# Kernel tuning notes

Measured on AMD Instinct MI355X. Metric: run time of the kernel, lower is better.

## Reference

```python
import jax, jax.numpy as jnp
import numpy as np

B, T, D = 2, 2048, 1024
NH, DH = 16, 64
DD_PAIRS = DH // 4          # 16
DD_DIM = DD_PAIRS * 2      # 32
FFN = (D * 8 // 3 + 7) // 8 * 8  # 2736
EPS = 1e-6


def rms_norm(x, w):
    # torch nn.RMSNorm: x / sqrt(mean(x^2) + eps) * w over last dim
    var = jnp.mean(jnp.square(x), axis=-1, keepdims=True)
    return x * jax.lax.rsqrt(var + EPS) * w


def apply_rotary(x, cos, sin):
    d = x.shape[-1]
    x1, x2 = x[..., : d // 2], x[..., d // 2 :]
    return jnp.concatenate([x1 * cos - x2 * sin, x2 * cos + x1 * sin], axis=-1)


def setup_inputs() -> dict:
    key = jax.random.key(0)
    ks = jax.random.split(key, 10)
    s = 0.02  # small init scale so activations stay sane
    # fixed RoPE tables: (1, T, 1, DH//2)
    inv_freq = 1.0 / (10000.0 ** (jnp.arange(DH // 2, dtype=jnp.float32) / (DH // 2)))
    ang = jnp.arange(T, dtype=jnp.float32)[:, None] * inv_freq[None, :]  # (T, 32)
    rope_cos = jnp.cos(ang)[None, :, None, :]
    rope_sin = jnp.sin(ang)[None, :, None, :]
    return {
        "x": jax.random.normal(ks[0], (B, T, D), jnp.float32),
        "rope_cos": rope_cos,
        "rope_sin": rope_sin,
        "lerp_w": jax.random.normal(ks[1], (D, D), jnp.float32) * s,
        "lerp_b": jnp.full((D,), -2.0, jnp.float32),
        "attn_norm_w": jnp.ones((D,), jnp.float32),
        "w_qkv": jax.random.normal(ks[2], (3 * D, D), jnp.float32) * s,
        "q_norm_w": jnp.ones((DH,), jnp.float32),
        "k_norm_w": jnp.ones((DH,), jnp.float32),
        "q_post_bias": jnp.ones((DH,), jnp.float32),
        "k_post_bias": jnp.ones((DH,), jnp.float32),
        "dd_w": jax.random.normal(ks[3], (NH * DD_PAIRS, D), jnp.float32) * s,
        "dd_b": jnp.zeros((NH * DD_PAIRS,), jnp.float32),
        "w_o": jax.random.normal(ks[4], (D, D), jnp.float32) * s,
        "mlp_norm_w": jnp.ones((D,), jnp.float32),
        "gate_w": jax.random.normal(ks[5], (FFN, D), jnp.float32) * s,
        "up_w": jax.random.normal(ks[6], (FFN, D), jnp.float32) * s,
        "down_w": jax.random.normal(ks[7], (D, FFN), jnp.float32) * s,
    }


def reference(x, rope_cos, rope_sin, lerp_w, lerp_b, attn_norm_w, w_qkv,
              q_norm_w, k_norm_w, q_post_bias, k_post_bias, dd_w, dd_b,
              w_o, mlp_norm_w, gate_w, up_w, down_w):
    # CausalLerp: x[t] <- (1-g)*x[t] + g*x[t-1], content-gated
    x_prev = jnp.pad(x[:, :-1], ((0, 0), (1, 0), (0, 0)))
    g = jax.nn.sigmoid(x @ lerp_w.T + lerp_b)
    x = (1.0 - g) * x + g * x_prev

    # Attention branch
    h = rms_norm(x, attn_norm_w)
    qkv = (h @ w_qkv.T).reshape(B, T, 3, NH, DH)
    q, k, v = qkv[:, :, 0], qkv[:, :, 1], qkv[:, :, 2]  # (B,T,NH,DH)
    q = rms_norm(q, q_norm_w) * q_post_bias
    k = rms_norm(k, k_norm_w) * k_post_bias

    # DD-RoPE angles: cumsum of learned deltas over time
    dd_angles = (x @ dd_w.T + dd_b).reshape(B, T, NH, DD_PAIRS)
    dd_angles = jnp.cumsum(dd_angles, axis=1)
    dd_cos, dd_sin = jnp.cos(dd_angles), jnp.sin(dd_angles)

    fp = DD_DIM // 2  # 16
    def hybrid(qk):
        fixed = apply_rotary(qk[..., :DD_DIM], rope_cos[..., :fp], rope_sin[..., :fp])
        dd = apply_rotary(qk[..., DD_DIM:], dd_cos, dd_sin)
        return jnp.concatenate([fixed, dd], axis=-1)

    q, k = hybrid(q), hybrid(k)

    # causal SDPA
    scale = 1.0 / jnp.sqrt(jnp.float32(DH))
    scores = jnp.einsum("bihd,bjhd->bhij", q, k) * scale  # (B,NH,T,T)
    causal = jnp.tril(jnp.ones((T, T), bool))
    scores = jnp.where(causal, scores, jnp.float32(-1e30))
    attn = jax.nn.softmax(scores, axis=-1)
    y = jnp.einsum("bhij,bjhd->bihd", attn, v).reshape(B, T, D)
    x = x + y @ w_o.T

    # SwiGLU MLP
    h = rms_norm(x, mlp_norm_w)
    x = x + (jax.nn.silu(h @ gate_w.T) * (h @ up_w.T)) @ down_w.T
    return x
```

## Files before the change

kernel.cpp:

```cpp
#include <hip/hip_runtime.h>

typedef unsigned short u16;
typedef __attribute__((ext_vector_type(8))) short short8;
typedef __attribute__((ext_vector_type(4))) short short4v;
typedef __attribute__((ext_vector_type(4))) float f32x4;
typedef __attribute__((ext_vector_type(4))) unsigned short u16x4;

static constexpr int TB   = 2;
static constexpr int TT   = 2048;
static constexpr int TD   = 1024;
static constexpr int TNH  = 16;
static constexpr int TDH  = 64;
static constexpr int TFFN = 2736;
static constexpr int TFFNP= 2752;
static constexpr int TBT  = TB * TT;

#define DEVI static __device__ __forceinline__

typedef __attribute__((address_space(1))) const unsigned int gas_t;
typedef __attribute__((address_space(3))) unsigned int las_t;
#define GLOAD16(src, dst) __builtin_amdgcn_global_load_lds((gas_t*)(src), (las_t*)(dst), 16, 0, 0)

DEVI u16 f2bf(float f) {
  union { float f; unsigned u; } v; v.f = f;
  unsigned r = v.u + 0x7FFFu + ((v.u >> 16) & 1u);
  return (u16)(r >> 16);
}
DEVI float bf2f(u16 u) {
  union { unsigned u; float f; } v; v.u = ((unsigned)u) << 16;
  return v.f;
}

DEVI unsigned cvtpk(float lo, float hi) {
  unsigned r;
  asm("v_cvt_pk_bf16_f32 %0, %1, %2" : "=v"(r) : "v"(lo), "v"(hi));
  return r;
}

#if __has_builtin(__builtin_amdgcn_mfma_f32_16x16x16bf16_1k)
#define MFMA16(a, b, c) __builtin_amdgcn_mfma_f32_16x16x16bf16_1k(a, b, c, 0, 0, 0)
#else
DEVI f32x4 mfma16_asm(short4v a, short4v b, f32x4 c) {
  asm("v_mfma_f32_16x16x16_bf16 %0, %1, %2, %0" : "+v"(c) : "v"(a), "v"(b));
  return c;
}
#define MFMA16(a, b, c) mfma16_asm(a, b, c)
#endif

__global__ void k_cvt(const float* __restrict__ s, u16* __restrict__ d, int n4) {
  int i = blockIdx.x * blockDim.x + threadIdx.x;
  int st = gridDim.x * blockDim.x;
  for (; i < n4; i += st) {
    float4 v = ((const float4*)s)[i];
    u16x4 u;
    u.x = f2bf(v.x); u.y = f2bf(v.y); u.z = f2bf(v.z); u.w = f2bf(v.w);
    ((u16x4*)d)[i] = u;
  }
}

__global__ void k_cvt_split3(const float* __restrict__ s, u16* __restrict__ d, int n) {
  int i = blockIdx.x * blockDim.x + threadIdx.x;
  int st = gridDim.x * blockDim.x;
  for (; i < n; i += st) {
    int c = i & 1023, r = i >> 10;
    float v = s[i];
    u16 h = f2bf(v);
    size_t base = (size_t)r * 3072 + c;
    d[base] = h;
    d[base + 1024] = h;
    d[base + 2048] = f2bf(v - bf2f(h));
  }
}

__global__ void k_cvt_pad(const float* __restrict__ s, u16* __restrict__ d,
                          int rows, int scol, int dcol) {
  int i = blockIdx.x * blockDim.x + threadIdx.x;
  int st = gridDim.x * blockDim.x;
  int n = rows * dcol;
  for (; i < n; i += st) {
    int c = i % dcol, r = i / dcol;
    d[i] = (c < scol) ? f2bf(s[(size_t)r * scol + c]) : (u16)0;
  }
}

__global__ __launch_bounds__(256) void k_rmsnorm(const float* __restrict__ x,
                                                 const float* __restrict__ w,
                                                 u16* __restrict__ o) {
  int row = blockIdx.x;
  float4 v = ((const float4*)(x + (size_t)row * TD))[threadIdx.x];
  float ss = v.x*v.x + v.y*v.y + v.z*v.z + v.w*v.w;
  #pragma unroll
  for (int m = 1; m < 64; m <<= 1) ss += __shfl_xor(ss, m);
  __shared__ float red[4];
  if ((threadIdx.x & 63) == 0) red[threadIdx.x >> 6] = ss;
  __syncthreads();
  float tot = red[0] + red[1] + red[2] + red[3];
  float sc = rsqrtf(tot * (1.0f / TD) + 1e-6f);
  float4 wv = ((const float4*)w)[threadIdx.x];
  u16x4 u;
  u.x = f2bf(v.x * sc * wv.x); u.y = f2bf(v.y * sc * wv.y);
  u.z = f2bf(v.z * sc * wv.z); u.w = f2bf(v.w * sc * wv.w);
  ((u16x4*)(o + (size_t)row * TD))[threadIdx.x] = u;
}

enum { EPI_LERP = 0, EPI_DD = 1, EPI_RESID = 2, EPI_B16 = 3 };

template<int BM, int EPI>
__global__ __launch_bounds__(256) void k_gemm_p4(
    const u16* __restrict__ A, const u16* __restrict__ B,
    int M, int N, int K,
    const float* __restrict__ aux0, const float* __restrict__ aux1,
    float* __restrict__ outF, u16* __restrict__ outB) {
  constexpr int MI = BM / 32;
  alignas(16) __shared__ u16 As[4][BM * 32];
  alignas(16) __shared__ u16 Bs[4][4096];
  const int lane = threadIdx.x & 63;
  const int w  = threadIdx.x >> 6;
  const int ln = lane & 15;
  const int g  = lane >> 4;
  const int swz = (ln >> 1) & 3;
  const int m0 = blockIdx.x * BM;
  const int n0 = blockIdx.y * 128;
  const int wm = (w >> 1) * (BM / 2);
  const int wn = (w & 1) * 64;

  const f32x4 fz = {0.f, 0.f, 0.f, 0.f};
  f32x4 acc[MI][4];
  #pragma unroll
  for (int mi = 0; mi < MI; mi++)
    #pragma unroll
    for (int ni = 0; ni < 4; ni++) acc[mi][ni] = fz;

  const int rsub = lane >> 2;
  const int csrc = (lane & 3) ^ ((lane >> 3) & 3);
  auto stage = [&](int buf, int kt) {
    const int k0 = kt * 32 + csrc * 8;
    if constexpr (BM == 128) {
      #pragma unroll
      for (int i = 0; i < 2; i++) {
        const int u = w + i * 4;
        int ar = m0 + u * 16 + rsub;
        GLOAD16(A + (size_t)ar * K + k0, &As[buf][u * 512]);
        int br = n0 + u * 16 + rsub; if (br > N - 1) br = N - 1;
        GLOAD16(B + (size_t)br * K + k0, &Bs[buf][u * 512]);
      }
    } else {
      int ar = m0 + w * 16 + rsub;
      GLOAD16(A + (size_t)ar * K + k0, &As[buf][w * 512]);
      #pragma unroll
      for (int i = 0; i < 2; i++) {
        const int u = w + i * 4;
        int br = n0 + u * 16 + rsub; if (br > N - 1) br = N - 1;
        GLOAD16(B + (size_t)br * K + k0, &Bs[buf][u * 512]);
      }
    }
  };

  const int nt = K / 32;
  stage(0, 0);
  stage(1, 1);
  for (int t = 0; t < nt; ++t) {
    const int cur = t & 3;
    if (t + 2 < nt) {
      stage((t + 2) & 3, t + 2);
      if constexpr (BM == 128) asm volatile("s_waitcnt vmcnt(8)" ::: "memory");
      else                     asm volatile("s_waitcnt vmcnt(6)" ::: "memory");
    } else if (t + 1 < nt) {
      if constexpr (BM == 128) asm volatile("s_waitcnt vmcnt(4)" ::: "memory");
      else                     asm volatile("s_waitcnt vmcnt(3)" ::: "memory");
    } else {
      asm volatile("s_waitcnt vmcnt(0)" ::: "memory");
    }
    __builtin_amdgcn_s_barrier();
    asm volatile("" ::: "memory");

    short8 af[MI], bfr[4];
    #pragma unroll
    for (int mi = 0; mi < MI; mi++)
      af[mi] = *(const short8*)&As[cur][(wm + mi * 16 + ln) * 32 + ((g ^ swz) << 3)];
    #pragma unroll
    for (int ni = 0; ni < 4; ni++)
      bfr[ni] = *(const short8*)&Bs[cur][(wn + ni * 16 + ln) * 32 + ((g ^ swz) << 3)];
    #pragma unroll
    for (int mi = 0; mi < MI; mi++)
      #pragma unroll
      for (int ni = 0; ni < 4; ni++)
        acc[mi][ni] = __builtin_amdgcn_mfma_f32_16x16x32_bf16(af[mi], bfr[ni], acc[mi][ni], 0, 0, 0);
  }

  #pragma unroll
  for (int mi = 0; mi < MI; mi++) {
    #pragma unroll
    for (int ni = 0; ni < 4; ni++) {
      int col = n0 + wn + ni * 16 + ln;
      #pragma unroll
      for (int r = 0; r < 4; r++) {
        int row = m0 + wm + mi * 16 + g * 4 + r;
        if (row >= M || col >= N) continue;
        float c = acc[mi][ni][r];
        size_t o = (size_t)row * N + col;
        if constexpr (EPI == EPI_LERP) {
          float gg = 1.0f / (1.0f + __expf(-(c + aux1[col])));
          float xv = aux0[o];
          float xp = (row & (TT - 1)) ? aux0[o - N] : 0.0f;
          float res = xv + gg * (xp - xv);
          outF[o] = res;
          u16 hi = f2bf(res);
          size_t xc = (size_t)row * 3072 + col;
          outB[xc] = hi;
          outB[xc + 2048] = hi;
          outB[xc + 1024] = f2bf(res - bf2f(hi));
        } else if constexpr (EPI == EPI_DD) {
          outF[o] = c + aux1[col];
        } else if constexpr (EPI == EPI_RESID) {
          outF[o] = aux0[o] + c;
        } else {
          outB[o] = f2bf(c);
        }
      }
    }
  }
}

__global__ __launch_bounds__(64) void k_csum1(const float* __restrict__ ang,
                                              float* __restrict__ seg) {
  int b = blockIdx.x, sg = blockIdx.y, q = threadIdx.x;
  const float4* p = (const float4*)(ang + ((size_t)(b * TT + sg * 16)) * 256) + q;
  float4 a = {0.f, 0.f, 0.f, 0.f};
  #pragma unroll 4
  for (int i = 0; i < 16; i++) {
    float4 v = p[(size_t)i * 64];
    a.x += v.x; a.y += v.y; a.z += v.z; a.w += v.w;
  }
  ((float4*)(seg + ((size_t)(b * 128 + sg)) * 256))[q] = a;
}

__global__ __launch_bounds__(512) void k_csum2(float* __restrict__ seg) {
  int b = threadIdx.x >> 8, col = threadIdx.x & 255;
  float acc = 0.f;
  for (int s = 0; s < 128; s++) {
    size_t o = ((size_t)(b * 128 + s)) * 256 + col;
    float v = seg[o];
    seg[o] = acc;
    acc += v;
  }
}

__global__ __launch_bounds__(64) void k_csum3(const float* __restrict__ ang,
                                              const float* __restrict__ seg,
                                              float* __restrict__ dc,
                                              float* __restrict__ ds) {
  int b = blockIdx.x, sg = blockIdx.y, q = threadIdx.x;
  size_t rowbase = ((size_t)(b * TT + sg * 16)) * 256;
  const float4* p = (const float4*)(ang + rowbase) + q;
  float4 a = ((const float4*)(seg + ((size_t)(b * 128 + sg)) * 256))[q];
  for (int i = 0; i < 16; i++) {
    float4 v = p[(size_t)i * 64];
    a.x += v.x; a.y += v.y; a.z += v.z; a.w += v.w;
    float4 c, s;
    c.x = cosf(a.x); s.x = sinf(a.x);
    c.y = cosf(a.y); s.y = sinf(a.y);
    c.z = cosf(a.z); s.z = sinf(a.z);
    c.w = cosf(a.w); s.w = sinf(a.w);
    ((float4*)(dc + rowbase))[(size_t)i * 64 + q] = c;
    ((float4*)(ds + rowbase))[(size_t)i * 64 + q] = s;
  }
}

__global__ __launch_bounds__(256) void k_qkv_post(
    const u16* __restrict__ qkv, const float* __restrict__ rc, const float* __restrict__ rs,
    const float* __restrict__ ddc, const float* __restrict__ dds,
    const float* __restrict__ qnw, const float* __restrict__ knw,
    const float* __restrict__ qpb, const float* __restrict__ kpb,
    u16* __restrict__ qb, u16* __restrict__ kb, u16* __restrict__ vT) {
  __shared__ u16 vt[64][72];
  const int lane = threadIdx.x & 63;
  const int w = threadIdx.x >> 6;
  const int bh = blockIdx.x, b = bh >> 4, h = bh & 15;
  const int t0 = blockIdx.y * 64;
  const float qsc = 0.125f * 1.44269504f;
  const float qw = qnw[lane] * qpb[lane];
  const float kw = knw[lane] * kpb[lane];
  const float sgn = (lane & 16) ? 1.0f : -1.0f;
  #pragma unroll 4
  for (int it = 0; it < 16; ++it) {
    int tl = w * 16 + it;
    int t = t0 + tl;
    size_t base = ((size_t)(b * TT + t)) * 3072 + h * 64 + lane;
    float q = bf2f(qkv[base]);
    float k = bf2f(qkv[base + 1024]);
    float v = bf2f(qkv[base + 2048]);
    float sq = q * q, sk = k * k;
    #pragma unroll
    for (int m = 1; m < 64; m <<= 1) { sq += __shfl_xor(sq, m); sk += __shfl_xor(sk, m); }
    q *= rsqrtf(sq * (1.0f / TDH) + 1e-6f) * qw;
    k *= rsqrtf(sk * (1.0f / TDH) + 1e-6f) * kw;
    float c, s;
    if (lane < 32) {
      c = rc[t * 32 + (lane & 15)];
      s = rs[t * 32 + (lane & 15)];
    } else {
      size_t ti = ((size_t)(b * TT + t)) * 256 + h * 16 + (lane & 15);
      c = ddc[ti];
      s = dds[ti];
    }
    float oq = __shfl_xor(q, 16);
    float ok = __shfl_xor(k, 16);
    float qr = (q * c + sgn * oq * s) * qsc;
    float kr = k * c + sgn * ok * s;
    size_t o = ((size_t)(bh * TT + t)) * 64 + lane;
    qb[o] = f2bf(qr);
    kb[o] = f2bf(kr);
    vt[lane][tl] = f2bf(v);
  }
  __syncthreads();
  int row = threadIdx.x >> 2, sg = threadIdx.x & 3;
  short8 v0 = *(const short8*)&vt[row][sg * 16];
  short8 v1 = *(const short8*)&vt[row][sg * 16 + 8];
  size_t o = ((size_t)(bh * 64 + row)) * TT + t0 + sg * 16;
  *(short8*)(vT + o) = v0;
  *(short8*)(vT + o + 8) = v1;
}

__global__ __launch_bounds__(256) void k_attn(
    const u16* __restrict__ qb, const u16* __restrict__ kb,
    const u16* __restrict__ vT, u16* __restrict__ y) {
  __shared__ u16 smem[16384];
  u16* Ks = smem;
  u16* Vs = smem + 8192;
  const int lane = threadIdx.x & 63;
  const int w = threadIdx.x >> 6;
  const int ln = lane & 15;
  const int g = lane >> 4;
  const int gh = g >> 1, gl = g & 1;
  const int bh = blockIdx.x;
  const int b = bh >> 4;
  const int by = 31 - (int)blockIdx.y;
  const int qt0 = by * 64 + w * 16;
  const u16* Q  = qb + (size_t)bh * TT * TDH;
  const u16* Kp = kb + (size_t)bh * TT * TDH;
  const u16* Vp = vT + (size_t)bh * TDH * TT;
  short8 qa0 = *(const short8*)(Q + (size_t)(qt0 + ln) * TDH + g * 8);
  short8 qa1 = *(const short8*)(Q + (size_t)(qt0 + ln) * TDH + 32 + g * 8);
  const f32x4 fz = {0.f, 0.f, 0.f, 0.f};
  f32x4 O[4];
  #pragma unroll
  for (int r = 0; r < 4; r++) O[r] = fz;
  float m = -1e30f, l = 0.0f;
  const int qlim = qt0 + ln;

  auto stage = [&](int buf, int j0) {
    #pragma unroll
    for (int i = 0; i < 2; i++) {
      int r = w * 16 + i * 8 + (lane >> 3);
      int c = (lane & 7) ^ (r & 7);
      GLOAD16(Kp + (size_t)(j0 + r) * TDH + c * 8, &Ks[buf * 4096 + w * 1024 + i * 512]);
      GLOAD16(Vp + (size_t)r * TT + j0 + c * 8, &Vs[buf * 4096 + w * 1024 + i * 512]);
    }
  };

  const int nt = by + 1;
  stage(0, 0);
  __syncthreads();
  for (int jt = 0; jt < nt; ++jt) {
    const int cur = jt & 1;
    if (jt + 1 < nt) stage(cur ^ 1, (jt + 1) * 64);
    const int j0 = jt * 64;
    f32x4 sc[4];
    #pragma unroll
    for (int c4 = 0; c4 < 4; c4++) {
      const u16* kr = Ks + cur * 4096 + (c4 * 16 + ln) * 64;
      short8 k0 = *(const short8*)(kr + ((g ^ (ln & 7)) * 8));
      short8 k1 = *(const short8*)(kr + (((g + 4) ^ (ln & 7)) * 8));
      f32x4 z = fz;
      z = __builtin_amdgcn_mfma_f32_16x16x32_bf16(k0, qa0, z, 0, 0, 0);
      z = __builtin_amdgcn_mfma_f32_16x16x32_bf16(k1, qa1, z, 0, 0, 0);
      sc[c4] = z;
    }
    if (jt == nt - 1) {
      #pragma unroll
      for (int c4 = 0; c4 < 4; c4++)
        #pragma unroll
        for (int r = 0; r < 4; r++)
          if (j0 + c4 * 16 + g * 4 + r > qlim) sc[c4][r] = -1e30f;
    }
    float pm = sc[0][0];
    #pragma unroll
    for (int c4 = 0; c4 < 4; c4++)
      #pragma unroll
      for (int r = 0; r < 4; r++) pm = fmaxf(pm, sc[c4][r]);
    pm = fmaxf(pm, __shfl_xor(pm, 16));
    pm = fmaxf(pm, __shfl_xor(pm, 32));
    bool grow = pm > m + 10.0f;
    if (__ballot(grow) != 0ull) {
      float mn = fmaxf(m, pm);
      float corr = exp2f(m - mn);
      #pragma unroll
      for (int dc = 0; dc < 4; dc++)
        #pragma unroll
        for (int r = 0; r < 4; r++) O[dc][r] *= corr;
      l *= corr;
      m = mn;
    }
    float rs_ = 0.0f;
    #pragma unroll
    for (int c4 = 0; c4 < 4; c4++)
      #pragma unroll
      for (int r = 0; r < 4; r++) {
        float pv = exp2f(sc[c4][r] - m);
        rs_ += pv;
        sc[c4][r] = pv;
      }
    rs_ += __shfl_xor(rs_, 16);
    rs_ += __shfl_xor(rs_, 32);
    l += rs_;
    short4v p4[4];
    #pragma unroll
    for (int c4 = 0; c4 < 4; c4++) {
      union { unsigned u[2]; short4v s; } pu;
      pu.u[0] = cvtpk(sc[c4][0], sc[c4][1]);
      pu.u[1] = cvtpk(sc[c4][2], sc[c4][3]);
      p4[c4] = pu.s;
    }
    #pragma unroll
    for (int dc = 0; dc < 4; dc++) {
      const int vrow = dc * 16 + ln;
      const u16* vbase = Vs + cur * 4096 + vrow * 64;
      #pragma unroll
      for (int c4 = 0; c4 < 4; c4++) {
        int chunk = (2 * c4 + gh) ^ (ln & 7);
        short4v va = *(const short4v*)(vbase + chunk * 8 + gl * 4);
        O[dc] = MFMA16(va, p4[c4], O[dc]);
      }
    }
    __syncthreads();
  }
  u16* ot = smem + w * 1152;
  float inv = 1.0f / l;
  #pragma unroll
  for (int dc = 0; dc < 4; dc++)
    #pragma unroll
    for (int r = 0; r < 4; r += 2) {
      unsigned pk = cvtpk(O[dc][r] * inv, O[dc][r + 1] * inv);
      *(unsigned*)(ot + ln * 72 + dc * 16 + g * 4 + r) = pk;
    }
  __syncthreads();
  int row = (threadIdx.x & 63) >> 2, sg = threadIdx.x & 3;
  u16* os = smem + w * 1152;
  short8 v0 = *(const short8*)(os + row * 72 + sg * 16);
  short8 v1 = *(const short8*)(os + row * 72 + sg * 16 + 8);
  size_t o = ((size_t)(b * TT + qt0 + row)) * TD + (bh & 15) * TDH + sg * 16;
  *(short8*)(y + o) = v0;
  *(short8*)(y + o + 8) = v1;
}

__global__ void k_swiglu(const u16* __restrict__ gu, u16* __restrict__ hb) {
  int i = blockIdx.x * blockDim.x + threadIdx.x;
  int n = TBT * 344;
  if (i >= n) return;
  int c8 = i % 344, r = i / 344;
  short8 o;
  if (c8 < 342) {
    short8 gv = *(const short8*)(gu + (size_t)r * 5472 + c8 * 8);
    short8 uv = *(const short8*)(gu + (size_t)r * 5472 + 2736 + c8 * 8);
    #pragma unroll
    for (int j = 0; j < 8; j++) {
      float gf = bf2f((u16)gv[j]);
      float uf = bf2f((u16)uv[j]);
      float sg = gf / (1.0f + __expf(-gf));
      o[j] = (short)f2bf(sg * uf);
    }
  } else {
    #pragma unroll
    for (int j = 0; j < 8; j++) o[j] = 0;
  }
  *(short8*)(hb + (size_t)r * TFFNP + c8 * 8) = o;
}

extern "C" void kernel_launch(void* const* d_in, const int* in_sizes, int n_in,
                              void* d_out, int out_size, void* d_ws, size_t ws_size,
                              hipStream_t stream) {
  const float* x      = (const float*)d_in[0];
  const float* ropec  = (const float*)d_in[1];
  const float* ropes  = (const float*)d_in[2];
  const float* lerp_w = (const float*)d_in[3];
  const float* lerp_b = (const float*)d_in[4];
  const float* anw    = (const float*)d_in[5];
  const float* w_qkv  = (const float*)d_in[6];
  const float* qnw    = (const float*)d_in[7];
  const float* knw    = (const float*)d_in[8];
  const float* qpb    = (const float*)d_in[9];
  const float* kpb    = (const float*)d_in[10];
  const float* dd_w   = (const float*)d_in[11];
  const float* dd_b   = (const float*)d_in[12];
  const float* w_o    = (const float*)d_in[13];
  const float* mnw    = (const float*)d_in[14];
  const float* gate_w = (const float*)d_in[15];
  const float* up_w   = (const float*)d_in[16];
  const float* down_w = (const float*)d_in[17];
  float* out = (float*)d_out;
  (void)in_sizes; (void)n_in; (void)out_size; (void)ws_size;

  char* ws = (char*)d_ws;
  size_t off = 0;
  auto alloc = [&](size_t bytes) -> char* {
    char* p = ws + off;
    off += (bytes + 255) & ~(size_t)255;
    return p;
  };

  char* segA = ws;
  u16* xb      = (u16*)alloc((size_t)TBT * TD * 2);
  u16* wb_lerp = (u16*)alloc((size_t)TD * TD * 2);
  u16* wb_qkv  = (u16*)alloc((size_t)3 * TD * TD * 2);
  u16* h_b     = (u16*)alloc((size_t)TBT * TD * 2);
  u16* xcat    = (u16*)alloc((size_t)TBT * 3072 * 2);
  u16* gu_b    = (u16*)segA;

  char* segF = ws + off;
  u16* qkv_b   = (u16*)alloc((size_t)TBT * 3 * TD * 2);
  u16* hb      = (u16*)segF;

  u16* wcat    = (u16*)alloc((size_t)256 * 3072 * 2);
  u16* wb_o    = (u16*)alloc((size_t)TD * TD * 2);
  u16* wb_gu   = (u16*)alloc((size_t)2 * TFFN * TD * 2);
  u16* wb_down = (u16*)alloc((size_t)TD * TFFNP * 2);
  float* x_mix = (float*)alloc((size_t)TBT * TD * 4);
  float* angles= (float*)alloc((size_t)TBT * 256 * 4);
  float* ddc   = (float*)alloc((size_t)TBT * 256 * 4);
  float* dds   = (float*)alloc((size_t)TBT * 256 * 4);
  float* segsum= (float*)alloc((size_t)2 * 128 * 256 * 4);
  u16* qb  = (u16*)alloc((size_t)TBT * TD * 2);
  u16* kb  = (u16*)alloc((size_t)TBT * TD * 2);
  u16* vT  = (u16*)alloc((size_t)TBT * TD * 2);
  u16* y_b = (u16*)alloc((size_t)TBT * TD * 2);
  float* x2  = (float*)alloc((size_t)TBT * TD * 4);
  u16* h2_b  = (u16*)alloc((size_t)TBT * TD * 2);

  k_cvt<<<dim3(1024), dim3(256), 0, stream>>>(x, xb, TBT * TD / 4);
  k_cvt<<<dim3(256),  dim3(256), 0, stream>>>(lerp_w, wb_lerp, TD * TD / 4);
  k_cvt<<<dim3(768),  dim3(256), 0, stream>>>(w_qkv, wb_qkv, 3 * TD * TD / 4);
  k_cvt_split3<<<dim3(256), dim3(256), 0, stream>>>(dd_w, wcat, 256 * TD);
  k_cvt<<<dim3(256),  dim3(256), 0, stream>>>(w_o, wb_o, TD * TD / 4);
  k_cvt<<<dim3(512),  dim3(256), 0, stream>>>(gate_w, wb_gu, TFFN * TD / 4);
  k_cvt<<<dim3(512),  dim3(256), 0, stream>>>(up_w, wb_gu + (size_t)TFFN * TD, TFFN * TD / 4);
  k_cvt_pad<<<dim3(512), dim3(256), 0, stream>>>(down_w, wb_down, TD, TFFN, TFFNP);

  k_gemm_p4<128, EPI_LERP><<<dim3(32, 8), dim3(256), 0, stream>>>(
      xb, wb_lerp, TBT, TD, TD, x, lerp_b, x_mix, xcat);

  k_rmsnorm<<<dim3(TBT), dim3(256), 0, stream>>>(x_mix, anw, h_b);

  k_gemm_p4<128, EPI_B16><<<dim3(32, 24), dim3(256), 0, stream>>>(
      h_b, wb_qkv, TBT, 3 * TD, TD, nullptr, nullptr, nullptr, qkv_b);

  k_gemm_p4<64, EPI_DD><<<dim3(64, 2), dim3(256), 0, stream>>>(
      xcat, wcat, TBT, 256, 3072, nullptr, dd_b, angles, nullptr);

  k_csum1<<<dim3(2, 128), dim3(64), 0, stream>>>(angles, segsum);
  k_csum2<<<dim3(1), dim3(512), 0, stream>>>(segsum);
  k_csum3<<<dim3(2, 128), dim3(64), 0, stream>>>(angles, segsum, ddc, dds);

  k_qkv_post<<<dim3(32, 32), dim3(256), 0, stream>>>(
      qkv_b, ropec, ropes, ddc, dds, qnw, knw, qpb, kpb, qb, kb, vT);

  k_attn<<<dim3(32, 32), dim3(256), 0, stream>>>(qb, kb, vT, y_b);

  k_gemm_p4<128, EPI_RESID><<<dim3(32, 8), dim3(256), 0, stream>>>(
      y_b, wb_o, TBT, TD, TD, x_mix, nullptr, x2, nullptr);

  k_rmsnorm<<<dim3(TBT), dim3(256), 0, stream>>>(x2, mnw, h2_b);
  k_gemm_p4<128, EPI_B16><<<dim3(32, 43), dim3(256), 0, stream>>>(
      h2_b, wb_gu, TBT, 2 * TFFN, TD, nullptr, nullptr, nullptr, gu_b);
  k_swiglu<<<dim3((TBT * 344 + 255) / 256), dim3(256), 0, stream>>>(gu_b, hb);
  k_gemm_p4<128, EPI_RESID><<<dim3(32, 8), dim3(256), 0, stream>>>(
      hb, wb_down, TBT, TD, TFFNP, x2, nullptr, out, nullptr);
}
```

Before: 570.5 us.

## Fuse conversion kernels, restructure GEMM pipeline, add MFMA priority hints, batch csum2 loads

Merges the eight fp32-to-bf16 conversion launches into one grid-stride kernel that dispatches on a flattened index. The GEMM main loop now processes two k-tiles per iteration with one barrier, issuing the next two stages before computing. It also raises wave priority around the MFMA blocks in the GEMM and attention. Separately, the serial segment scan in csum2 loads sixteen values at a time to hide memory latency. These target launch overhead, barrier count and latency stalls, but the branchy fused conversion and the new wait placement could reduce efficiency or change overlap.

```diff
diff --git a/kernel.cpp b/kernel.cpp
--- a/kernel.cpp
+++ b/kernel.cpp
@@ -47,39 +47,62 @@
 #define MFMA16(a, b, c) mfma16_asm(a, b, c)
 #endif
 
-__global__ void k_cvt(const float* __restrict__ s, u16* __restrict__ d, int n4) {
+__global__ void k_cvt_all(const float* __restrict__ x,  const float* __restrict__ lw,
+                          const float* __restrict__ wq, const float* __restrict__ wo,
+                          const float* __restrict__ gw, const float* __restrict__ uw,
+                          const float* __restrict__ dw, const float* __restrict__ ddw,
+                          u16* __restrict__ xb,  u16* __restrict__ wbl,
+                          u16* __restrict__ wbq, u16* __restrict__ wbo,
+                          u16* __restrict__ wbgu, u16* __restrict__ wbd,
+                          u16* __restrict__ wcat) {
+  constexpr int U0 = TBT * TD / 4;
+  constexpr int U1 = TD * TD / 4;
+  constexpr int U2 = 3 * TD * TD / 4;
+  constexpr int U3 = TD * TD / 4;
+  constexpr int U4 = TFFN * TD / 4;
+  constexpr int U5 = TFFN * TD / 4;
+  constexpr int U6 = TD * (TFFNP / 4);
+  constexpr int U7 = 256 * TD / 4;
+  constexpr int P1 = U0, P2 = P1 + U1, P3 = P2 + U2, P4 = P3 + U3;
+  constexpr int P5 = P4 + U4, P6 = P5 + U5, P7 = P6 + U6, PT = P7 + U7;
   int i = blockIdx.x * blockDim.x + threadIdx.x;
   int st = gridDim.x * blockDim.x;
-  for (; i < n4; i += st) {
-    float4 v = ((const float4*)s)[i];
-    u16x4 u;
-    u.x = f2bf(v.x); u.y = f2bf(v.y); u.z = f2bf(v.z); u.w = f2bf(v.w);
-    ((u16x4*)d)[i] = u;
-  }
-}
-
-__global__ void k_cvt_split3(const float* __restrict__ s, u16* __restrict__ d, int n) {
-  int i = blockIdx.x * blockDim.x + threadIdx.x;
-  int st = gridDim.x * blockDim.x;
-  for (; i < n; i += st) {
-    int c = i & 1023, r = i >> 10;
-    float v = s[i];
-    u16 h = f2bf(v);
-    size_t base = (size_t)r * 3072 + c;
-    d[base] = h;
-    d[base + 1024] = h;
-    d[base + 2048] = f2bf(v - bf2f(h));
-  }
-}
-
-__global__ void k_cvt_pad(const float* __restrict__ s, u16* __restrict__ d,
-                          int rows, int scol, int dcol) {
-  int i = blockIdx.x * blockDim.x + threadIdx.x;
-  int st = gridDim.x * blockDim.x;
-  int n = rows * dcol;
-  for (; i < n; i += st) {
-    int c = i % dcol, r = i / dcol;
-    d[i] = (c < scol) ? f2bf(s[(size_t)r * scol + c]) : (u16)0;
+  for (; i < PT; i += st) {
+    if (i < P6) {
+      const float* s; u16* d; int j;
+      if (i < P1)      { s = x;  d = xb;  j = i; }
+      else if (i < P2) { s = lw; d = wbl; j = i - P1; }
+      else if (i < P3) { s = wq; d = wbq; j = i - P2; }
+      else if (i < P4) { s = wo; d = wbo; j = i - P3; }
+      else if (i < P5) { s = gw; d = wbgu; j = i - P4; }
+      else             { s = uw; d = wbgu + (size_t)TFFN * TD; j = i - P5; }
+      float4 v = ((const float4*)s)[j];
+      u16x4 u;
+      u.x = f2bf(v.x); u.y = f2bf(v.y); u.z = f2bf(v.z); u.w = f2bf(v.w);
+      ((u16x4*)d)[j] = u;
+    } else if (i < P7) {
+      int j = i - P6;
+      int c4 = j % (TFFNP / 4), r = j / (TFFNP / 4);
+      u16x4 u;
+      if (c4 < TFFN / 4) {
+        const float* sp = dw + (size_t)r * TFFN + c4 * 4;
+        u.x = f2bf(sp[0]); u.y = f2bf(sp[1]); u.z = f2bf(sp[2]); u.w = f2bf(sp[3]);
+      } else { u.x = u.y = u.z = u.w = 0; }
+      ((u16x4*)wbd)[(size_t)r * (TFFNP / 4) + c4] = u;
+    } else {
+      int j = i - P7;
+      int c = (j & 255) * 4, r = j >> 8;
+      float4 v = *(const float4*)(ddw + (size_t)r * 1024 + c);
+      size_t base = (size_t)r * 3072 + c;
+      #pragma unroll
+      for (int e = 0; e < 4; e++) {
+        float f = (e == 0) ? v.x : (e == 1) ? v.y : (e == 2) ? v.z : v.w;
+        u16 h = f2bf(f);
+        wcat[base + e] = h;
+        wcat[base + 1024 + e] = h;
+        wcat[base + 2048 + e] = f2bf(f - bf2f(h));
+      }
+    }
   }
 }
 
@@ -156,36 +179,42 @@
     }
   };
 
+  auto compute = [&](int cur) {
+    short8 af[MI], bfr[4];
+    #pragma unroll
+    for (int mi = 0; mi < MI; mi++)
+      af[mi] = *(const short8*)&As[cur][(wm + mi * 16 + ln) * 32 + ((g ^ swz) << 3)];
+    #pragma unroll
+    for (int ni = 0; ni < 4; ni++)
+      bfr[ni] = *(const short8*)&Bs[cur][(wn + ni * 16 + ln) * 32 + ((g ^ swz) << 3)];
+    __builtin_amdgcn_s_setprio(1);
+    #pragma unroll
+    for (int mi = 0; mi < MI; mi++)
+      #pragma unroll
+      for (int ni = 0; ni < 4; ni++)
+        acc[mi][ni] = __builtin_amdgcn_mfma_f32_16x16x32_bf16(af[mi], bfr[ni], acc[mi][ni], 0, 0, 0);
+    __builtin_amdgcn_s_setprio(0);
+  };
+
   const int nt = K / 32;
   stage(0, 0);
   stage(1, 1);
-  for (int t = 0; t < nt; ++t) {
-    const int cur = t & 3;
-    if (t + 2 < nt) {
-      stage((t + 2) & 3, t + 2);
+  for (int t = 0; t < nt; t += 2) {
+    if constexpr (BM == 128) asm volatile("s_waitcnt vmcnt(4)" ::: "memory");
+    else                     asm volatile("s_waitcnt vmcnt(3)" ::: "memory");
+    __builtin_amdgcn_s_barrier();
+    asm volatile("" ::: "memory");
+    const bool more = (t + 2 < nt);
+    if (more) { stage((t + 2) & 3, t + 2); stage((t + 3) & 3, t + 3); }
+    compute(t & 3);
+    if (more) {
       if constexpr (BM == 128) asm volatile("s_waitcnt vmcnt(8)" ::: "memory");
       else                     asm volatile("s_waitcnt vmcnt(6)" ::: "memory");
-    } else if (t + 1 < nt) {
-      if constexpr (BM == 128) asm volatile("s_waitcnt vmcnt(4)" ::: "memory");
-      else                     asm volatile("s_waitcnt vmcnt(3)" ::: "memory");
     } else {
       asm volatile("s_waitcnt vmcnt(0)" ::: "memory");
     }
-    __builtin_amdgcn_s_barrier();
     asm volatile("" ::: "memory");
-
-    short8 af[MI], bfr[4];
-    #pragma unroll
-    for (int mi = 0; mi < MI; mi++)
-      af[mi] = *(const short8*)&As[cur][(wm + mi * 16 + ln) * 32 + ((g ^ swz) << 3)];
-    #pragma unroll
-    for (int ni = 0; ni < 4; ni++)
-      bfr[ni] = *(const short8*)&Bs[cur][(wn + ni * 16 + ln) * 32 + ((g ^ swz) << 3)];
-    #pragma unroll
-    for (int mi = 0; mi < MI; mi++)
-      #pragma unroll
-      for (int ni = 0; ni < 4; ni++)
-        acc[mi][ni] = __builtin_amdgcn_mfma_f32_16x16x32_bf16(af[mi], bfr[ni], acc[mi][ni], 0, 0, 0);
+    compute((t + 1) & 3);
   }
 
   #pragma unroll
@@ -237,12 +266,18 @@
 
 __global__ __launch_bounds__(512) void k_csum2(float* __restrict__ seg) {
   int b = threadIdx.x >> 8, col = threadIdx.x & 255;
-  float acc = 0.f;
-  for (int s = 0; s < 128; s++) {
-    size_t o = ((size_t)(b * 128 + s)) * 256 + col;
-    float v = seg[o];
-    seg[o] = acc;
-    acc += v;
+  float run = 0.f;
+  for (int s0 = 0; s0 < 128; s0 += 16) {
+    float v[16];
+    #pragma unroll
+    for (int i = 0; i < 16; i++)
+      v[i] = seg[((size_t)(b * 128 + s0 + i)) * 256 + col];
+    #pragma unroll
+    for (int i = 0; i < 16; i++) {
+      float t = v[i];
+      seg[((size_t)(b * 128 + s0 + i)) * 256 + col] = run;
+      run += t;
+    }
   }
 }
 
@@ -367,6 +402,7 @@
     if (jt + 1 < nt) stage(cur ^ 1, (jt + 1) * 64);
     const int j0 = jt * 64;
     f32x4 sc[4];
+    __builtin_amdgcn_s_setprio(1);
     #pragma unroll
     for (int c4 = 0; c4 < 4; c4++) {
       const u16* kr = Ks + cur * 4096 + (c4 * 16 + ln) * 64;
@@ -377,6 +413,7 @@
       z = __builtin_amdgcn_mfma_f32_16x16x32_bf16(k1, qa1, z, 0, 0, 0);
       sc[c4] = z;
     }
+    __builtin_amdgcn_s_setprio(0);
     if (jt == nt - 1) {
       #pragma unroll
       for (int c4 = 0; c4 < 4; c4++)
@@ -422,6 +459,7 @@
       pu.u[1] = cvtpk(sc[c4][2], sc[c4][3]);
       p4[c4] = pu.s;
     }
+    __builtin_amdgcn_s_setprio(1);
     #pragma unroll
     for (int dc = 0; dc < 4; dc++) {
       const int vrow = dc * 16 + ln;
@@ -433,6 +471,7 @@
         O[dc] = MFMA16(va, p4[c4], O[dc]);
       }
     }
+    __builtin_amdgcn_s_setprio(0);
     __syncthreads();
   }
   u16* ot = smem + w * 1152;
@@ -537,14 +576,9 @@
   float* x2  = (float*)alloc((size_t)TBT * TD * 4);
   u16* h2_b  = (u16*)alloc((size_t)TBT * TD * 2);
 
-  k_cvt<<<dim3(1024), dim3(256), 0, stream>>>(x, xb, TBT * TD / 4);
-  k_cvt<<<dim3(256),  dim3(256), 0, stream>>>(lerp_w, wb_lerp, TD * TD / 4);
-  k_cvt<<<dim3(768),  dim3(256), 0, stream>>>(w_qkv, wb_qkv, 3 * TD * TD / 4);
-  k_cvt_split3<<<dim3(256), dim3(256), 0, stream>>>(dd_w, wcat, 256 * TD);
-  k_cvt<<<dim3(256),  dim3(256), 0, stream>>>(w_o, wb_o, TD * TD / 4);
-  k_cvt<<<dim3(512),  dim3(256), 0, stream>>>(gate_w, wb_gu, TFFN * TD / 4);
-  k_cvt<<<dim3(512),  dim3(256), 0, stream>>>(up_w, wb_gu + (size_t)TFFN * TD, TFFN * TD / 4);
-  k_cvt_pad<<<dim3(512), dim3(256), 0, stream>>>(down_w, wb_down, TD, TFFN, TFFNP);
+  k_cvt_all<<<dim3(2048), dim3(256), 0, stream>>>(
+      x, lerp_w, w_qkv, w_o, gate_w, up_w, down_w, dd_w,
+      xb, wb_lerp, wb_qkv, wb_o, wb_gu, wb_down, wcat);
 
   k_gemm_p4<128, EPI_LERP><<<dim3(32, 8), dim3(256), 0, stream>>>(
       xb, wb_lerp, TBT, TD, TD, x, lerp_b, x_mix, xcat);
```

New measurement: 546.3 us. 1.04x faster.
